# Kernel optimization log

Hardware: AMD Instinct MI355X
Metric: run time of the kernel (lower is better)

Reference implementation:

```python
import jax, jax.numpy as jnp
import numpy as np
from jax import lax

# ---- constants from init_kwargs (train_coefficients=False -> scalar coeffs) ----
TAU_M, TAU_S = 4.0, 1.0
A1 = float(np.exp(-1.0 / TAU_M) + np.exp(-1.0 / TAU_S))          # IIR feedback coeff 1
A2 = float(-np.exp(-1.0 / TAU_M - 1.0 / TAU_S))                  # IIR feedback coeff 2
ETA = TAU_M / TAU_S
V0 = float(ETA ** (ETA / (ETA - 1.0)) / (ETA - 1.0))             # PSP normalization
SIGMA = float(np.exp(-1.0 / TAU_M))                              # membrane decay
LENGTH = 100
V_TH = 1.0


def dual_exp_iir(x_seq):
    """Dual-exponential synapse as 2nd-order IIR. x_seq: [T, B, F].
    y[t] = A1*y[t-1] + A2*y[t-2] + V0*x[t], zero init states."""
    z = jnp.zeros_like(x_seq[0])
    def step(carry, x_t):
        s1, s2 = carry
        y = A1 * s1 + A2 * s2 + V0 * x_t
        return (y, s1), y
    _, out = lax.scan(step, (z, z), x_seq)
    return out


def spike_fn(v):
    return (v > V_TH).astype(v.dtype)


def neuron_layer(x_seq, w, b):
    """LIF neurons with membrane filter (reset-to-zero on spike).
    x_seq: [T, B, Fin]; w: [Fout, Fin]; b: [Fout]. Returns spikes [T, B, Fout]."""
    cur = jnp.einsum('tbi,oi->tbo', x_seq, w) + b  # batched GEMM over all timesteps
    z = jnp.zeros_like(cur[0])
    def step(carry, c_t):
        v, prev_s = carry
        v_new = SIGMA * v * (1.0 - prev_s) + c_t
        s = spike_fn(v_new)
        return (v_new, s), s
    _, spikes = lax.scan(step, (z, z), cur)
    return spikes


def setup_inputs() -> dict:
    key = jax.random.key(0)
    ks = jax.random.split(key, 7)
    B = 256
    inputs = jax.random.uniform(ks[0], (B, 784), dtype=jnp.float32)
    def lin(k, fo, fi):
        return jax.random.normal(k, (fo, fi), dtype=jnp.float32) / np.sqrt(fi)
    return {
        'inputs': inputs,
        'w1': lin(ks[1], 500, 784), 'b1': jnp.zeros((500,), jnp.float32),
        'w2': lin(ks[2], 500, 500), 'b2': jnp.zeros((500,), jnp.float32),
        'w3': lin(ks[3], 10, 500),  'b3': jnp.zeros((10,), jnp.float32),
    }


def reference(inputs, w1, b1, w2, b2, w3, b3):
    # expand_along_time: [B, 784] -> [T, B, 784] (time-major internally)
    x = jnp.broadcast_to(inputs[None, :, :], (LENGTH,) + inputs.shape)
    h = dual_exp_iir(x)
    s1 = neuron_layer(h, w1, b1)
    h = dual_exp_iir(s1)
    s2 = neuron_layer(h, w2, b2)
    h = dual_exp_iir(s2)
    s3 = neuron_layer(h, w3, b3)            # [T, B, 10]
    return jnp.transpose(s3, (1, 2, 0))     # [B, 10, T] to match torch layout
```

## Files before the change

kernel.cpp:

```cpp
#include <hip/hip_runtime.h>
#include <cstdint>
#include <cstddef>

using f16x8 = __attribute__((ext_vector_type(8))) _Float16;
using f32x4 = __attribute__((ext_vector_type(4))) float;

static constexpr float cA1  =  1.1466802242428472f;
static constexpr float cA2  = -0.2865047968601901f;
static constexpr float cV0  =  2.1165347359575991f;
static constexpr float cSIG =  0.7788007830714049f;

#define TSTEPS 100
#define BATCH  256
#define KPAD   512
#define MROWS  (TSTEPS * BATCH)
#define KS1    7

__device__ __forceinline__ void gload_lds16(const void* g, void* l) {
  __builtin_amdgcn_global_load_lds(
      (void __attribute__((address_space(1)))*)g,
      (void __attribute__((address_space(3)))*)l, 16, 0, 0);
}

__global__ void split_w2(const float* __restrict__ w2,
                         _Float16* __restrict__ Wh, _Float16* __restrict__ Wl) {
  int idx = blockIdx.x * 256 + threadIdx.x;
  int n = idx >> 9, k = idx & 511;
  float x = (n < 500 && k < 500) ? w2[n * 500 + k] : 0.f;
  _Float16 h = (_Float16)x;
  float r = x - (float)h;
  _Float16 l = (_Float16)(r * 4096.f);
  Wh[idx] = h; Wl[idx] = l;
}

#define BM1 64
#define BN1 64
#define BK1 32
#define LDT1 68

__global__ __launch_bounds__(256)
void gemm1_splitk(const float* __restrict__ A, const float* __restrict__ B,
                  float* __restrict__ P) {
  constexpr int M = 256, N = 500, K = 784;
  __shared__ float As[BK1][LDT1];
  __shared__ float Bs[BK1][LDT1];
  const int tid = threadIdx.x;
  const int bm  = blockIdx.y * BM1;
  const int bn  = blockIdx.x * BN1;
  const int ks  = blockIdx.z;
  const int k_begin = ks * 128;
  const int k_end   = (k_begin + 128 < K) ? k_begin + 128 : K;
  const int tr  = tid >> 4;
  const int tc  = tid & 15;
  float acc[4][4] = {{0.f}};

  for (int k0 = k_begin; k0 < k_end; k0 += BK1) {
#pragma unroll
    for (int i = 0; i < 2; ++i) {
      const int t = tid + i * 256;
      const int r = t >> 3;
      const int c = (t & 7) << 2;
      const int gk = k0 + c;
      float4 va = make_float4(0.f, 0.f, 0.f, 0.f);
      const int gm = bm + r;
      if (gm < M && gk < k_end) {
        if (gk + 3 < k_end) va = *(const float4*)(A + (size_t)gm * K + gk);
        else {
          const float* p = A + (size_t)gm * K;
          va.x = p[gk];
          if (gk + 1 < k_end) va.y = p[gk + 1];
          if (gk + 2 < k_end) va.z = p[gk + 2];
        }
      }
      As[c + 0][r] = va.x; As[c + 1][r] = va.y;
      As[c + 2][r] = va.z; As[c + 3][r] = va.w;
      float4 vb = make_float4(0.f, 0.f, 0.f, 0.f);
      const int gn = bn + r;
      if (gn < N && gk < k_end) {
        if (gk + 3 < k_end) vb = *(const float4*)(B + (size_t)gn * K + gk);
        else {
          const float* p = B + (size_t)gn * K;
          vb.x = p[gk];
          if (gk + 1 < k_end) vb.y = p[gk + 1];
          if (gk + 2 < k_end) vb.z = p[gk + 2];
        }
      }
      Bs[c + 0][r] = vb.x; Bs[c + 1][r] = vb.y;
      Bs[c + 2][r] = vb.z; Bs[c + 3][r] = vb.w;
    }
    __syncthreads();
#pragma unroll
    for (int kk = 0; kk < BK1; ++kk) {
      const float4 a = *(const float4*)&As[kk][tr * 4];
      const float4 b = *(const float4*)&Bs[kk][tc * 4];
      acc[0][0] += a.x * b.x; acc[0][1] += a.x * b.y; acc[0][2] += a.x * b.z; acc[0][3] += a.x * b.w;
      acc[1][0] += a.y * b.x; acc[1][1] += a.y * b.y; acc[1][2] += a.y * b.z; acc[1][3] += a.y * b.w;
      acc[2][0] += a.z * b.x; acc[2][1] += a.z * b.y; acc[2][2] += a.z * b.z; acc[2][3] += a.z * b.w;
      acc[3][0] += a.w * b.x; acc[3][1] += a.w * b.y; acc[3][2] += a.w * b.z; acc[3][3] += a.w * b.w;
    }
    __syncthreads();
  }
#pragma unroll
  for (int i = 0; i < 4; ++i) {
    const int m = bm + tr * 4 + i;
#pragma unroll
    for (int j = 0; j < 4; ++j) {
      const int n = bn + tc * 4 + j;
      if (n < N) P[((size_t)ks * 256 + m) * 512 + n] = acc[i][j];
    }
  }
}

__global__ __launch_bounds__(256)
void layer1_split(const float* __restrict__ P,
                  const float* __restrict__ b1,
                  _Float16* __restrict__ Ah,
                  _Float16* __restrict__ Al) {
  int idx = blockIdx.x * 256 + threadIdx.x;
  int b = idx >> 9, o = idx & 511;
  if (o >= 500) {
    for (int t = 0; t < TSTEPS; ++t) {
      size_t off = (size_t)(t * BATCH + b) * KPAD + o;
      Ah[off] = (_Float16)0; Al[off] = (_Float16)0;
    }
    return;
  }
  float g = 0.f;
  for (int ks = 0; ks < KS1; ++ks)
    g += P[((size_t)ks * 256 + b) * 512 + o];
  const float bb = b1[o];
  float v = 0.f, sp = 0.f, y1 = 0.f, y2 = 0.f;
  float c1 = 0.f, c2 = 0.f;
  for (int t = 0; t < TSTEPS; ++t) {
    float c = cA1 * c1 + cA2 * c2 + cV0; c2 = c1; c1 = c;
    float cur = c * g + bb;
    float vv = cSIG * v * (1.f - sp) + cur;
    float s = (vv > 1.f) ? 1.f : 0.f;
    v = vv; sp = s;
    float y = cA1 * y1 + cA2 * y2 + cV0 * s;
    y2 = y1; y1 = y;
    _Float16 h = (_Float16)y;
    float r = y - (float)h;
    size_t off = (size_t)(t * BATCH + b) * KPAD + o;
    Ah[off] = h;
    Al[off] = (_Float16)(r * 4096.f);
  }
}

__global__ __launch_bounds__(512, 4)
void gemm2_f16(const _Float16* __restrict__ Ah, const _Float16* __restrict__ Al,
               const _Float16* __restrict__ Bh, const _Float16* __restrict__ Bl,
               const float* __restrict__ bias, float* __restrict__ C) {
  constexpr int K = KPAD;
  __shared__ char smem[4 * 16384];
  char* sAh = smem;
  char* sAl = smem + 16384;
  char* sBh = smem + 32768;
  char* sBl = smem + 49152;

  const int tid  = threadIdx.x;
  const int lane = tid & 63;
  const int wid  = tid >> 6;
  const int wr   = wid >> 2;
  const int wc   = wid & 3;
  const int orig = blockIdx.x + blockIdx.y * 2;
  const int wg   = (orig & 7) * 50 + (orig >> 3);
  const int bm   = (wg >> 1) * 128;
  const int bxl  = wg & 1;

  const int lrow = lane & 15;
  const int lkc  = lane >> 4;

#pragma unroll 1
  for (int job = 0; job < 2; ++job) {
    const int bn = (bxl * 2 + job) * 128;

    f32x4 acc0[4][2], acc1[4][2];
#pragma unroll
    for (int m = 0; m < 4; ++m)
#pragma unroll
      for (int n = 0; n < 2; ++n) {
        acc0[m][n] = (f32x4){0.f, 0.f, 0.f, 0.f};
        acc1[m][n] = (f32x4){0.f, 0.f, 0.f, 0.f};
      }

    for (int k0 = 0; k0 < K; k0 += 64) {
#pragma unroll
      for (int i = 0; i < 2; ++i) {
        int l = i * 8192 + tid * 16;
        int row = l >> 7;
        int chunk = ((l >> 4) & 7) ^ (row & 7);
        size_t ga = (size_t)(bm + row) * K + k0 + chunk * 8;
        gload_lds16(Ah + ga, sAh + l);
        gload_lds16(Al + ga, sAl + l);
      }
#pragma unroll
      for (int i = 0; i < 2; ++i) {
        int l = i * 8192 + tid * 16;
        int row = l >> 7;
        int chunk = ((l >> 4) & 7) ^ (row & 7);
        size_t gb = (size_t)(bn + row) * K + k0 + chunk * 8;
        gload_lds16(Bh + gb, sBh + l);
        gload_lds16(Bl + gb, sBl + l);
      }
      __syncthreads();

#pragma unroll
      for (int kh = 0; kh < 2; ++kh) {
        const int kc = kh * 4 + lkc;
        f16x8 ah[4], al[4];
#pragma unroll
        for (int m = 0; m < 4; ++m) {
          int row = wr * 64 + m * 16 + lrow;
          int off = row * 128 + ((kc ^ (row & 7)) << 4);
          ah[m] = *(const f16x8*)(sAh + off);
          al[m] = *(const f16x8*)(sAl + off);
        }
#pragma unroll
        for (int n = 0; n < 2; ++n) {
          int row = wc * 32 + n * 16 + lrow;
          int off = row * 128 + ((kc ^ (row & 7)) << 4);
          f16x8 bh = *(const f16x8*)(sBh + off);
          f16x8 bl = *(const f16x8*)(sBl + off);
#pragma unroll
          for (int m = 0; m < 4; ++m) {
            acc0[m][n] = __builtin_amdgcn_mfma_f32_16x16x32_f16(ah[m], bh, acc0[m][n], 0, 0, 0);
            acc1[m][n] = __builtin_amdgcn_mfma_f32_16x16x32_f16(ah[m], bl, acc1[m][n], 0, 0, 0);
            acc1[m][n] = __builtin_amdgcn_mfma_f32_16x16x32_f16(al[m], bh, acc1[m][n], 0, 0, 0);
          }
        }
      }
      __syncthreads();
    }

#pragma unroll
    for (int m = 0; m < 4; ++m) {
      int gm0 = bm + wr * 64 + m * 16 + (lane >> 4) * 4;
#pragma unroll
      for (int n = 0; n < 2; ++n) {
        int gn = bn + wc * 32 + n * 16 + (lane & 15);
        float bs = (gn < 500) ? bias[gn] : 0.f;
#pragma unroll
        for (int r = 0; r < 4; ++r)
          C[(size_t)(gm0 + r) * KPAD + gn] =
              acc0[m][n][r] + 0.000244140625f * acc1[m][n][r] + bs;
      }
    }
  }
}

__global__ __launch_bounds__(256)
void lif_mid(float* __restrict__ q) {
  int idx = blockIdx.x * 256 + threadIdx.x;
  int b = idx >> 9, o = idx & 511;
  if (o >= 500) return;
  float v = 0.f, sp = 0.f, y1 = 0.f, y2 = 0.f;
  for (int t = 0; t < TSTEPS; ++t) {
    size_t off = (size_t)(t * BATCH + b) * KPAD + o;
    float qv = q[off];
    float vv = cSIG * v * (1.f - sp) + qv;
    float s = (vv > 1.f) ? 1.f : 0.f;
    v = vv; sp = s;
    float y = cA1 * y1 + cA2 * y2 + cV0 * s;
    y2 = y1; y1 = y;
    q[off] = y;
  }
}

__global__ __launch_bounds__(256)
void gemm3_wave(const float* __restrict__ y, const float* __restrict__ w3,
                float* __restrict__ q3) {
  __shared__ float ws3[10 * 500];
  for (int i = threadIdx.x; i < 5000; i += 256) ws3[i] = w3[i];
  __syncthreads();
  const int wid = threadIdx.x >> 6, lane = threadIdx.x & 63;
  const int m = blockIdx.x * 4 + wid;
  float p[10];
#pragma unroll
  for (int o = 0; o < 10; ++o) p[o] = 0.f;
  for (int k = lane; k < 500; k += 64) {
    float h = y[(size_t)m * KPAD + k];
#pragma unroll
    for (int o = 0; o < 10; ++o) p[o] += h * ws3[o * 500 + k];
  }
#pragma unroll
  for (int o = 0; o < 10; ++o) {
    float v = p[o];
    for (int off = 32; off; off >>= 1) v += __shfl_down(v, off, 64);
    if (lane == 0) q3[(size_t)m * 10 + o] = v;
  }
}

__global__ __launch_bounds__(64)
void lif_out3(const float* __restrict__ q,
              const float* __restrict__ b3,
              float* __restrict__ out) {
  int idx = blockIdx.x * 64 + threadIdx.x;
  if (idx >= BATCH * 10) return;
  int b = idx / 10, o = idx - b * 10;
  float bb = b3[o];
  float v = 0.f, sp = 0.f;
  for (int t = 0; t < TSTEPS; ++t) {
    float cur = q[(size_t)(t * BATCH + b) * 10 + o] + bb;
    float vv = cSIG * v * (1.f - sp) + cur;
    float s = (vv > 1.f) ? 1.f : 0.f;
    v = vv; sp = s;
    out[(size_t)b * 1000 + (size_t)o * 100 + t] = s;
  }
}

extern "C" void kernel_launch(void* const* d_in, const int* in_sizes, int n_in,
                              void* d_out, int out_size, void* d_ws, size_t ws_size,
                              hipStream_t stream) {
  const float* inputs = (const float*)d_in[0];
  const float* w1 = (const float*)d_in[1];
  const float* b1 = (const float*)d_in[2];
  const float* w2 = (const float*)d_in[3];
  const float* b2 = (const float*)d_in[4];
  const float* w3 = (const float*)d_in[5];
  const float* b3 = (const float*)d_in[6];
  float* out = (float*)d_out;

  char* ws = (char*)d_ws;
  _Float16* w2h = (_Float16*)ws; ws += 512 * 512 * 2;
  _Float16* w2l = (_Float16*)ws; ws += 512 * 512 * 2;
  float* P1 = (float*)ws;        ws += (size_t)KS1 * 256 * 512 * 4;
  float* q2 = (float*)ws;        ws += (size_t)MROWS * KPAD * 4;
  float* q3 = (float*)ws;        ws += (size_t)MROWS * 10 * 4;
  _Float16* Ah = (_Float16*)ws;  ws += (size_t)MROWS * KPAD * 2;
  _Float16* Al = (_Float16*)ws;  ws += (size_t)MROWS * KPAD * 2;

  split_w2<<<dim3(512 * 512 / 256), dim3(256), 0, stream>>>(w2, w2h, w2l);

  gemm1_splitk<<<dim3(8, 4, KS1), dim3(256), 0, stream>>>(inputs, w1, P1);
  layer1_split<<<dim3(BATCH * 512 / 256), dim3(256), 0, stream>>>(P1, b1, Ah, Al);

  gemm2_f16<<<dim3(2, 200), dim3(512), 0, stream>>>(Ah, Al, w2h, w2l, b2, q2);
  lif_mid<<<dim3(BATCH * 512 / 256), dim3(256), 0, stream>>>(q2);

  gemm3_wave<<<dim3(MROWS / 4), dim3(256), 0, stream>>>(q2, w3, q3);
  lif_out3<<<dim3((BATCH * 10 + 63) / 64), dim3(64), 0, stream>>>(q3, b3, out);
}
```

Measured before the change: 147.5 us.

## Double-buffer gemm2 LDS tiles and give each block all four N-tiles

Restructures gemm2 so each workgroup owns one 128-row M tile and loops over all four N tiles, which cuts the grid from 400 to 200 blocks. LDS is double-buffered (128 KB), and the global-to-LDS load of the next K step is issued before computing on the current buffer, so one barrier per step replaces two. The aim is to hide global-load latency behind MFMA work and to reuse the A tile across N. In exchange, the larger LDS footprint and launch bounds of 2 lower occupancy, and 200 blocks may leave some of the 256 CUs idle.

```diff
diff --git a/kernel.cpp b/kernel.cpp
--- a/kernel.cpp
+++ b/kernel.cpp
@@ -147,34 +147,45 @@
   }
 }
 
-__global__ __launch_bounds__(512, 4)
+__global__ __launch_bounds__(512, 2)
 void gemm2_f16(const _Float16* __restrict__ Ah, const _Float16* __restrict__ Al,
                const _Float16* __restrict__ Bh, const _Float16* __restrict__ Bl,
                const float* __restrict__ bias, float* __restrict__ C) {
-  constexpr int K = KPAD;
-  __shared__ char smem[4 * 16384];
-  char* sAh = smem;
-  char* sAl = smem + 16384;
-  char* sBh = smem + 32768;
-  char* sBl = smem + 49152;
-
+  __shared__ char smem[2][4][16384];
   const int tid  = threadIdx.x;
   const int lane = tid & 63;
   const int wid  = tid >> 6;
   const int wr   = wid >> 2;
   const int wc   = wid & 3;
-  const int orig = blockIdx.x + blockIdx.y * 2;
-  const int wg   = (orig & 7) * 50 + (orig >> 3);
-  const int bm   = (wg >> 1) * 128;
-  const int bxl  = wg & 1;
-
+  const int g    = blockIdx.x;
+  const int wg   = (g & 7) * 25 + (g >> 3);
+  const int bm   = wg * 128;
   const int lrow = lane & 15;
   const int lkc  = lane >> 4;
 
+  auto stage = [&](int buf, int step) {
+    const int k0 = (step & 7) * 64;
+    const int bn = (step >> 3) * 128;
+#pragma unroll
+    for (int i = 0; i < 2; ++i) {
+      const int l = i * 8192 + tid * 16;
+      const int row = l >> 7;
+      const int chunk = ((l >> 4) & 7) ^ (row & 7);
+      const size_t ga = (size_t)(bm + row) * KPAD + k0 + chunk * 8;
+      const size_t gb = (size_t)(bn + row) * KPAD + k0 + chunk * 8;
+      gload_lds16(Ah + ga, &smem[buf][0][l]);
+      gload_lds16(Al + ga, &smem[buf][1][l]);
+      gload_lds16(Bh + gb, &smem[buf][2][l]);
+      gload_lds16(Bl + gb, &smem[buf][3][l]);
+    }
+  };
+
+  stage(0, 0);
+  asm volatile("s_waitcnt vmcnt(0)" ::: "memory");
+  __builtin_amdgcn_s_barrier();
+
 #pragma unroll 1
-  for (int job = 0; job < 2; ++job) {
-    const int bn = (bxl * 2 + job) * 128;
-
+  for (int job = 0; job < 4; ++job) {
     f32x4 acc0[4][2], acc1[4][2];
 #pragma unroll
     for (int m = 0; m < 4; ++m)
@@ -184,42 +195,31 @@
         acc1[m][n] = (f32x4){0.f, 0.f, 0.f, 0.f};
       }
 
-    for (int k0 = 0; k0 < K; k0 += 64) {
-#pragma unroll
-      for (int i = 0; i < 2; ++i) {
-        int l = i * 8192 + tid * 16;
-        int row = l >> 7;
-        int chunk = ((l >> 4) & 7) ^ (row & 7);
-        size_t ga = (size_t)(bm + row) * K + k0 + chunk * 8;
-        gload_lds16(Ah + ga, sAh + l);
-        gload_lds16(Al + ga, sAl + l);
-      }
-#pragma unroll
-      for (int i = 0; i < 2; ++i) {
-        int l = i * 8192 + tid * 16;
-        int row = l >> 7;
-        int chunk = ((l >> 4) & 7) ^ (row & 7);
-        size_t gb = (size_t)(bn + row) * K + k0 + chunk * 8;
-        gload_lds16(Bh + gb, sBh + l);
-        gload_lds16(Bl + gb, sBl + l);
-      }
-      __syncthreads();
-
+#pragma unroll 1
+    for (int T = 0; T < 8; ++T) {
+      const int step = job * 8 + T;
+      const int cur  = step & 1;
+      if (step < 31) stage(cur ^ 1, step + 1);
+
+      const char* sAh = smem[cur][0];
+      const char* sAl = smem[cur][1];
+      const char* sBh = smem[cur][2];
+      const char* sBl = smem[cur][3];
 #pragma unroll
       for (int kh = 0; kh < 2; ++kh) {
         const int kc = kh * 4 + lkc;
         f16x8 ah[4], al[4];
 #pragma unroll
         for (int m = 0; m < 4; ++m) {
-          int row = wr * 64 + m * 16 + lrow;
-          int off = row * 128 + ((kc ^ (row & 7)) << 4);
+          const int row = wr * 64 + m * 16 + lrow;
+          const int off = row * 128 + ((kc ^ (row & 7)) << 4);
           ah[m] = *(const f16x8*)(sAh + off);
           al[m] = *(const f16x8*)(sAl + off);
         }
 #pragma unroll
         for (int n = 0; n < 2; ++n) {
-          int row = wc * 32 + n * 16 + lrow;
-          int off = row * 128 + ((kc ^ (row & 7)) << 4);
+          const int row = wc * 32 + n * 16 + lrow;
+          const int off = row * 128 + ((kc ^ (row & 7)) << 4);
           f16x8 bh = *(const f16x8*)(sBh + off);
           f16x8 bl = *(const f16x8*)(sBl + off);
 #pragma unroll
@@ -230,16 +230,18 @@
           }
         }
       }
-      __syncthreads();
-    }
-
+      asm volatile("s_waitcnt vmcnt(0)" ::: "memory");
+      __builtin_amdgcn_s_barrier();
+    }
+
+    const int bn = job * 128;
 #pragma unroll
     for (int m = 0; m < 4; ++m) {
-      int gm0 = bm + wr * 64 + m * 16 + (lane >> 4) * 4;
+      const int gm0 = bm + wr * 64 + m * 16 + (lane >> 4) * 4;
 #pragma unroll
       for (int n = 0; n < 2; ++n) {
-        int gn = bn + wc * 32 + n * 16 + (lane & 15);
-        float bs = (gn < 500) ? bias[gn] : 0.f;
+        const int gn = bn + wc * 32 + n * 16 + (lane & 15);
+        const float bs = (gn < 500) ? bias[gn] : 0.f;
 #pragma unroll
         for (int r = 0; r < 4; ++r)
           C[(size_t)(gm0 + r) * KPAD + gn] =
@@ -335,7 +337,7 @@
   gemm1_splitk<<<dim3(8, 4, KS1), dim3(256), 0, stream>>>(inputs, w1, P1);
   layer1_split<<<dim3(BATCH * 512 / 256), dim3(256), 0, stream>>>(P1, b1, Ah, Al);
 
-  gemm2_f16<<<dim3(2, 200), dim3(512), 0, stream>>>(Ah, Al, w2h, w2l, b2, q2);
+  gemm2_f16<<<dim3(200), dim3(512), 0, stream>>>(Ah, Al, w2h, w2l, b2, q2);
   lif_mid<<<dim3(BATCH * 512 / 256), dim3(256), 0, stream>>>(q2);
 
   gemm3_wave<<<dim3(MROWS / 4), dim3(256), 0, stream>>>(q2, w3, q3);
```

New measurement: 148.1 us. About the same (+0.4%).

## Fuse layer-2 LIF, layer-3 GEMV and output LIF into one per-batch kernel

Applied to the files above, without the earlier changes.

Replaces three kernels (lif_mid, gemm3_wave, lif_out3) with one kernel that runs one block per batch element. Each block walks time, computes the layer-2 spike and IIR output into shared memory, takes the 10-wide dot product against w3 held in shared memory, and runs the output LIF in place. This drops the write-back of y into q2, the re-read by gemm3, the q3 buffer and two launches. In exchange the kernel runs only 256 blocks with two __syncthreads per timestep, so the serial time loop may limit parallelism and latency hiding.

```diff
diff --git a/kernel.cpp b/kernel.cpp
--- a/kernel.cpp
+++ b/kernel.cpp
@@ -249,63 +249,58 @@
   }
 }
 
-__global__ __launch_bounds__(256)
-void lif_mid(float* __restrict__ q) {
-  int idx = blockIdx.x * 256 + threadIdx.x;
-  int b = idx >> 9, o = idx & 511;
-  if (o >= 500) return;
+__global__ __launch_bounds__(640)
+void lif23(const float* __restrict__ q2, const float* __restrict__ w3,
+           const float* __restrict__ b3, float* __restrict__ out) {
+  __shared__ float ws3[10 * 512];
+  __shared__ float yb[512];
+  __shared__ float dotbuf[16];
+  const int tid = threadIdx.x;
+  const int b   = blockIdx.x;
+  for (int i = tid; i < 5120; i += 640) {
+    int j = i >> 9, k = i & 511;
+    ws3[i] = (k < 500) ? w3[j * 500 + k] : 0.f;
+  }
+  const int o = tid;
+  const int wv = tid >> 6, lane = tid & 63;
   float v = 0.f, sp = 0.f, y1 = 0.f, y2 = 0.f;
+  float vo = 0.f, spo = 0.f;
+  const float bb3 = (tid < 10) ? b3[tid] : 0.f;
+  float qcur = (o < 512) ? q2[(size_t)b * KPAD + o] : 0.f;
+  __syncthreads();
+
   for (int t = 0; t < TSTEPS; ++t) {
-    size_t off = (size_t)(t * BATCH + b) * KPAD + o;
-    float qv = q[off];
-    float vv = cSIG * v * (1.f - sp) + qv;
-    float s = (vv > 1.f) ? 1.f : 0.f;
-    v = vv; sp = s;
-    float y = cA1 * y1 + cA2 * y2 + cV0 * s;
-    y2 = y1; y1 = y;
-    q[off] = y;
-  }
-}
-
-__global__ __launch_bounds__(256)
-void gemm3_wave(const float* __restrict__ y, const float* __restrict__ w3,
-                float* __restrict__ q3) {
-  __shared__ float ws3[10 * 500];
-  for (int i = threadIdx.x; i < 5000; i += 256) ws3[i] = w3[i];
-  __syncthreads();
-  const int wid = threadIdx.x >> 6, lane = threadIdx.x & 63;
-  const int m = blockIdx.x * 4 + wid;
-  float p[10];
-#pragma unroll
-  for (int o = 0; o < 10; ++o) p[o] = 0.f;
-  for (int k = lane; k < 500; k += 64) {
-    float h = y[(size_t)m * KPAD + k];
-#pragma unroll
-    for (int o = 0; o < 10; ++o) p[o] += h * ws3[o * 500 + k];
-  }
-#pragma unroll
-  for (int o = 0; o < 10; ++o) {
-    float v = p[o];
-    for (int off = 32; off; off >>= 1) v += __shfl_down(v, off, 64);
-    if (lane == 0) q3[(size_t)m * 10 + o] = v;
-  }
-}
-
-__global__ __launch_bounds__(64)
-void lif_out3(const float* __restrict__ q,
-              const float* __restrict__ b3,
-              float* __restrict__ out) {
-  int idx = blockIdx.x * 64 + threadIdx.x;
-  if (idx >= BATCH * 10) return;
-  int b = idx / 10, o = idx - b * 10;
-  float bb = b3[o];
-  float v = 0.f, sp = 0.f;
-  for (int t = 0; t < TSTEPS; ++t) {
-    float cur = q[(size_t)(t * BATCH + b) * 10 + o] + bb;
-    float vv = cSIG * v * (1.f - sp) + cur;
-    float s = (vv > 1.f) ? 1.f : 0.f;
-    v = vv; sp = s;
-    out[(size_t)b * 1000 + (size_t)o * 100 + t] = s;
+    float yv = 0.f;
+    if (o < 500) {
+      float vv = cSIG * v * (1.f - sp) + qcur;
+      float s = (vv > 1.f) ? 1.f : 0.f;
+      v = vv; sp = s;
+      float y = cA1 * y1 + cA2 * y2 + cV0 * s;
+      y2 = y1; y1 = y;
+      yv = y;
+    }
+    if (o < 512) yb[o] = yv;
+    float qnext = 0.f;
+    if (o < 512 && t + 1 < TSTEPS)
+      qnext = q2[(size_t)((t + 1) * BATCH + b) * KPAD + o];
+    __syncthreads();
+
+    float p = 0.f;
+#pragma unroll
+    for (int kk = 0; kk < 8; ++kk)
+      p += yb[lane + kk * 64] * ws3[wv * 512 + lane + kk * 64];
+    for (int off2 = 32; off2; off2 >>= 1) p += __shfl_down(p, off2, 64);
+    if (lane == 0) dotbuf[wv] = p;
+    __syncthreads();
+
+    if (tid < 10) {
+      float cur = dotbuf[tid] + bb3;
+      float vv = cSIG * vo * (1.f - spo) + cur;
+      float s = (vv > 1.f) ? 1.f : 0.f;
+      vo = vv; spo = s;
+      out[(size_t)b * 1000 + tid * 100 + t] = s;
+    }
+    qcur = qnext;
   }
 }
 
@@ -326,7 +321,6 @@
   _Float16* w2l = (_Float16*)ws; ws += 512 * 512 * 2;
   float* P1 = (float*)ws;        ws += (size_t)KS1 * 256 * 512 * 4;
   float* q2 = (float*)ws;        ws += (size_t)MROWS * KPAD * 4;
-  float* q3 = (float*)ws;        ws += (size_t)MROWS * 10 * 4;
   _Float16* Ah = (_Float16*)ws;  ws += (size_t)MROWS * KPAD * 2;
   _Float16* Al = (_Float16*)ws;  ws += (size_t)MROWS * KPAD * 2;
 
@@ -336,8 +330,6 @@
   layer1_split<<<dim3(BATCH * 512 / 256), dim3(256), 0, stream>>>(P1, b1, Ah, Al);
 
   gemm2_f16<<<dim3(2, 200), dim3(512), 0, stream>>>(Ah, Al, w2h, w2l, b2, q2);
-  lif_mid<<<dim3(BATCH * 512 / 256), dim3(256), 0, stream>>>(q2);
-
-  gemm3_wave<<<dim3(MROWS / 4), dim3(256), 0, stream>>>(q2, w3, q3);
-  lif_out3<<<dim3((BATCH * 10 + 63) / 64), dim3(64), 0, stream>>>(q3, b3, out);
-}
+
+  lif23<<<dim3(BATCH), dim3(640), 0, stream>>>(q2, w3, b3, out);
+}
```

Result: slower. 164.7 us (+11.6%).
